# Performance work log

Measured on AMD Instinct MI355X. Metric: run time of the kernel, lower is better.

Reference implementation:

```python
import jax, jax.numpy as jnp
import numpy as np

# Module hyper-parameters (from init_kwargs)
NDIM = 2
KSIZE = [3, 3]            # must be odd per ConvSP checks
DILATION = [0.05, 0.05]
RADIUS = 0.1
C_IN, C_OUT = 64, 64
B, N = 2, 2048


def _offsets():
    # Kernel-cell center offsets relative to the particle, row-major over dims
    # (matches the cartesian ordering of the original C extension).
    axes = [(np.arange(k) - (k - 1) / 2.0) * d for k, d in zip(KSIZE, DILATION)]
    grids = np.meshgrid(*axes, indexing='ij')
    return np.stack([g.reshape(-1) for g in grids], axis=-1).astype(np.float32)  # [ncells, D]


def setup_inputs() -> dict:
    key = jax.random.key(0)
    k1, k2, k3, k4, k5, k6 = jax.random.split(key, 6)
    pos = jax.random.uniform(k1, (B, N, NDIM), dtype=jnp.float32)          # coords in [0,1]^D
    invmass = jax.random.uniform(k2, (B, N), dtype=jnp.float32) * 0.9 + 0.1  # avoid 1/0
    locs = jnp.concatenate([pos, invmass[..., None]], axis=-1)             # [B,N,D+1]
    data = jax.random.normal(k3, (B, C_IN, N), dtype=jnp.float32)
    density = jax.random.uniform(k4, (B, N), dtype=jnp.float32) + 0.5      # strictly positive
    ncells = int(np.prod(KSIZE))
    weight = jax.random.normal(k5, (C_OUT, C_IN, ncells), dtype=jnp.float32) * 0.05
    bias = jax.random.normal(k6, (C_OUT,), dtype=jnp.float32) * 0.05
    return {"locs": locs, "data": data, "density": density, "weight": weight, "bias": bias}


def _convsp(locs, data, density, weight, bias):
    # SPH interpolation at each kernel-cell query point r_{i,k} = x_i + off_k:
    #   field[b,c,i,k] = sum_j (m_j / rho_j) * data[b,c,j] * W(|x_j - r_{i,k}|, RADIUS)
    # with m_j = 1/invmass_j, then a 1x1-style contraction with weight over (c,k).
    pos = locs[..., :NDIM]                               # [B,N,D]
    invmass = locs[..., NDIM]                            # [B,N]
    coef = 1.0 / (invmass * density)                     # m_j / rho_j, [B,N]
    dcoef = data * coef[:, None, :]                      # [B,C,N]
    diff = pos[:, :, None, :] - pos[:, None, :, :]       # x_i - x_j, [B,N,N,D]
    r2 = RADIUS * RADIUS
    knorm = 315.0 / (64.0 * np.pi * RADIUS ** 9)         # poly6 smoothing kernel norm
    offs = _offsets()                                    # [ncells, D]
    bsz, n = pos.shape[0], pos.shape[1]
    out = jnp.broadcast_to(bias[None, :, None], (bsz, weight.shape[0], n))
    for k in range(offs.shape[0]):                       # fixed small ncells=9 loop
        # |x_j - x_i - off| == |(x_i - x_j) + off|
        d2 = jnp.sum((diff + offs[k]) ** 2, axis=-1)     # [B,N,N] (i = query, j = neighbor)
        w = jnp.where(d2 < r2, (r2 - d2) ** 3, 0.0) * knorm
        field = jnp.einsum('bcj,bij->bci', dcoef, w)     # gather-weighted average
        out = out + jnp.einsum('oc,bci->boi', weight[:, :, k], field)
    return out


def reference(locs, data, density, weight, bias):
    return _convsp(locs, data, density, weight, bias)
```

## Files before the change

kernel.cpp:

```cpp
#include <hip/hip_runtime.h>
#include <hip/hip_bf16.h>
#include <stdint.h>

#define BATCH 2
#define NPTS  2048
#define CIN   64
#define COUT  64
#define NCELL 9

#define KNORM 1.5666851e9f
#define R2 0.01f

typedef __attribute__((ext_vector_type(8))) __bf16 bf16x8;
typedef __attribute__((ext_vector_type(4))) float  f32x4;

union B8 { uint4 u; bf16x8 v; };

typedef __attribute__((address_space(3))) uint8_t        lds_t;
typedef const __attribute__((address_space(1))) uint8_t  glb_t;

static __device__ __forceinline__ unsigned pk2(float a, float b) {
    union { __hip_bfloat162 h; unsigned u; } cv;
    cv.h = __float22bfloat162_rn(make_float2(a, b));
    return cv.u;
}


__global__ __launch_bounds__(256) void prep_kernel(
    const float* __restrict__ locs, const float* __restrict__ data,
    const float* __restrict__ density, const float* __restrict__ weight,
    const float* __restrict__ bias,
    float2* __restrict__ posT, uint16_t* __restrict__ dC,
    uint16_t* __restrict__ WB, float* __restrict__ out)
{
    const int tid = threadIdx.x;
    const int g = blockIdx.x;
    if (g < 256) {
        int e = g * 256 + tid;
        int j4 = e & 511, bc = e >> 9;
        int b = bc >> 6;
        float4 dv = *(const float4*)(data + bc * 2048 + j4 * 4);
        float4 de = *(const float4*)(density + b * 2048 + j4 * 4);
        int jb = (b * 2048 + j4 * 4) * 3 + 2;
        float m0 = locs[jb], m1 = locs[jb + 3], m2 = locs[jb + 6], m3 = locs[jb + 9];
        float v0 = dv.x / (m0 * de.x);
        float v1 = dv.y / (m1 * de.y);
        float v2 = dv.z / (m2 * de.z);
        float v3 = dv.w / (m3 * de.w);
        *(uint2*)(dC + bc * 2048 + j4 * 4) = make_uint2(pk2(v0, v1), pk2(v2, v3));
    } else if (g < 272) {
        int jj = (g - 256) * 256 + tid;
        posT[jj] = make_float2(locs[jj * 3], locs[jj * 3 + 1]);
    } else if (g < 272 + NCELL) {
        int cell = g - 272;
        for (int it = 0; it < 16; it++) {
            int e = it * 256 + tid;
            int ks = e >> 11, ob = (e >> 9) & 3, lane = (e >> 3) & 63, jj = e & 7;
            int o = ob * 16 + (lane & 15);
            int c = ks * 32 + ((lane >> 4) & 3) * 8 + jj;
            union { __hip_bfloat16 h; uint16_t u; } cv;
            cv.h = __float2bfloat16(weight[(o * 64 + c) * 9 + cell]);
            WB[cell * 4096 + e] = cv.u;
        }
    } else {
        const int gb = g - (272 + NCELL);
#pragma unroll
        for (int r = 0; r < 2; r++) {
            int e4 = (gb * 512 + r * 256 + tid) * 4;
            float bv = bias[(e4 >> 11) & 63];
            *(float4*)(out + e4) = make_float4(bv, bv, bv, bv);
        }
    }
}

__global__ __launch_bounds__(256, 4) void conv_kernel(
    const float2* __restrict__ posT, const uint16_t* __restrict__ dC,
    const uint16_t* __restrict__ WB, float* __restrict__ out)
{
    __shared__ uint16_t db[2][2048];
    __shared__ float    sft[4 * 16 * 68];

    const int tid  = threadIdx.x;
    const int lane = tid & 63;
    const int wid  = tid >> 6;
    const int cl   = lane & 15;
    const int quad = lane >> 4;
    const int bx   = blockIdx.x;
    const int b    = bx >> 9;
    const int i0   = ((bx >> 2) & 127) * 16;
    const int jh   = bx & 3;
    const int jb0  = jh * 512;

    const int c0 = (wid == 0) ? 0 : (1 + wid * 2);
    const int nc = (wid == 0) ? 3 : 2;
    float oxr[3], oyr[3];
#pragma unroll
    for (int ci = 0; ci < 3; ci++) {
        int k = c0 + (ci < nc ? ci : 0);
        oxr[ci] = (float)(k / 3 - 1) * 0.05f;
        oyr[ci] = (float)(k % 3 - 1) * 0.05f;
    }

    const float2 pI = posT[b * 2048 + i0 + cl];

    f32x4 acc[3][4];
#pragma unroll
    for (int ci = 0; ci < 3; ci++)
#pragma unroll
        for (int nb = 0; nb < 4; nb++) acc[ci][nb] = (f32x4){0.f, 0.f, 0.f, 0.f};

    const uint16_t* srcbase =
        dC + (b * 64 + wid * 16 + (lane >> 2)) * 2048 + jb0 + (lane & 3) * 8;

#define STAGE(n, buf)                                                         \
    __builtin_amdgcn_global_load_lds((glb_t*)(srcbase + (n) * 32),            \
                                     (lds_t*)(&db[buf][wid * 512]), 16, 0, 0)

    STAGE(0, 0);

    for (int n = 0; n < 16; n++) {
        __syncthreads();
        if (n < 15) STAGE(n + 1, (n + 1) & 1);
        const int buf = n & 1;

        B8 bf[4];
#pragma unroll
        for (int nb = 0; nb < 4; nb++)
            bf[nb].u = *(const uint4*)&db[buf][(nb * 16 + cl) * 32 + quad * 8];

        const float4* pp = (const float4*)(posT + b * 2048 + jb0 + n * 32 + quad * 8);
        float4 q0 = pp[0], q1 = pp[1], q2 = pp[2], q3 = pp[3];
        float dxv[8], dyv[8];
        dxv[0] = pI.x - q0.x; dyv[0] = pI.y - q0.y;
        dxv[1] = pI.x - q0.z; dyv[1] = pI.y - q0.w;
        dxv[2] = pI.x - q1.x; dyv[2] = pI.y - q1.y;
        dxv[3] = pI.x - q1.z; dyv[3] = pI.y - q1.w;
        dxv[4] = pI.x - q2.x; dyv[4] = pI.y - q2.y;
        dxv[5] = pI.x - q2.z; dyv[5] = pI.y - q2.w;
        dxv[6] = pI.x - q3.x; dyv[6] = pI.y - q3.y;
        dxv[7] = pI.x - q3.z; dyv[7] = pI.y - q3.w;

#pragma unroll
        for (int ci = 0; ci < 3; ci++) {
            if (ci < nc) {
                float ox = oxr[ci], oy = oyr[ci];
                float w[8];
#pragma unroll
                for (int p = 0; p < 8; p++) {
                    float ax = dxv[p] + ox;
                    float sx = fmaf(-ax, ax, R2);
                    float ay = dyv[p] + oy;
                    float t  = fmaf(-ay, ay, sx);
                    float mt = fmaxf(t, 0.0f);
                    w[p] = (mt * mt) * (mt * KNORM);
                }
                B8 af;
                af.u = make_uint4(pk2(w[0], w[1]), pk2(w[2], w[3]),
                                  pk2(w[4], w[5]), pk2(w[6], w[7]));
#pragma unroll
                for (int nb = 0; nb < 4; nb++)
                    acc[ci][nb] = __builtin_amdgcn_mfma_f32_16x16x32_bf16(
                        af.v, bf[nb].v, acc[ci][nb], 0, 0, 0);
            }
        }
    }

    float* scr = &sft[wid * (16 * 68)];
    f32x4 acc2[4];
#pragma unroll
    for (int ob = 0; ob < 4; ob++) acc2[ob] = (f32x4){0.f, 0.f, 0.f, 0.f};

#pragma unroll
    for (int ci = 0; ci < 3; ci++) {
        if (ci < nc) {
#pragma unroll
            for (int nb = 0; nb < 4; nb++)
#pragma unroll
                for (int r = 0; r < 4; r++)
                    scr[(quad * 4 + r) * 68 + nb * 16 + cl] = acc[ci][nb][r];
            int k = c0 + ci;
#pragma unroll
            for (int ks = 0; ks < 2; ks++) {
                const float* fp = &scr[cl * 68 + ks * 32 + quad * 8];
                float4 lo = *(const float4*)fp;
                float4 hi = *(const float4*)(fp + 4);
                B8 af;
                af.u = make_uint4(pk2(lo.x, lo.y), pk2(lo.z, lo.w),
                                  pk2(hi.x, hi.y), pk2(hi.z, hi.w));
#pragma unroll
                for (int ob = 0; ob < 4; ob++) {
                    B8 wf;
                    wf.u = *(const uint4*)(WB + k * 4096 + (ks * 4 + ob) * 512 + lane * 8);
                    acc2[ob] = __builtin_amdgcn_mfma_f32_16x16x32_bf16(
                        af.v, wf.v, acc2[ob], 0, 0, 0);
                }
            }
        }
    }

    __syncthreads();
#pragma unroll
    for (int ob = 0; ob < 4; ob++)
#pragma unroll
        for (int r = 0; r < 4; r++)
            scr[(quad * 4 + r) * 68 + ob * 16 + cl] = acc2[ob][r];
    __syncthreads();

    {
        const int i  = tid & 15;
        const int og = tid >> 4;
        float4 s0 = *(const float4*)&sft[0 * 1088 + i * 68 + og * 4];
        float4 s1 = *(const float4*)&sft[1 * 1088 + i * 68 + og * 4];
        float4 s2 = *(const float4*)&sft[2 * 1088 + i * 68 + og * 4];
        float4 s3 = *(const float4*)&sft[3 * 1088 + i * 68 + og * 4];
        float v0 = s0.x + s1.x + s2.x + s3.x;
        float v1 = s0.y + s1.y + s2.y + s3.y;
        float v2 = s0.z + s1.z + s2.z + s3.z;
        float v3 = s0.w + s1.w + s2.w + s3.w;
        float* ob_ = out + (b * 64 + og * 4) * 2048 + i0 + i;
        unsafeAtomicAdd(ob_ + 0 * 2048, v0);
        unsafeAtomicAdd(ob_ + 1 * 2048, v1);
        unsafeAtomicAdd(ob_ + 2 * 2048, v2);
        unsafeAtomicAdd(ob_ + 3 * 2048, v3);
    }
#undef STAGE
}

extern "C" void kernel_launch(void* const* d_in, const int* in_sizes, int n_in,
                              void* d_out, int out_size, void* d_ws, size_t ws_size,
                              hipStream_t stream)
{
    const float* locs    = (const float*)d_in[0];
    const float* data    = (const float*)d_in[1];
    const float* density = (const float*)d_in[2];
    const float* weight  = (const float*)d_in[3];
    const float* bias    = (const float*)d_in[4];
    float* out = (float*)d_out;

    float2*   posT = (float2*)d_ws;
    uint16_t* dC   = (uint16_t*)((char*)d_ws + 32768);
    uint16_t* WB   = (uint16_t*)((char*)d_ws + 32768 + 524288);

    prep_kernel<<<272 + NCELL + 128, 256, 0, stream>>>(
        locs, data, density, weight, bias, posT, dC, WB, out);
    conv_kernel<<<BATCH * 128 * 4, 256, 0, stream>>>(posT, dC, WB, out);
}
```

Before: 91.83 us.

## Split neighbor range across waves with all nine cells per wave, drop LDS staging

Restructures the conv kernel so each wave handles all 9 kernel cells over its own slice of the neighbor range, instead of splitting cells across waves. The x-direction distance terms are computed once and shared by three cells each. Neighbor data is now read straight from global memory into registers with a one-step software prefetch, replacing the LDS double buffer with global_load_lds and its per-step barriers. The grid is halved to 2 j-chunks per i-tile and launch bounds drop to 2 blocks per SM. In exchange, register pressure rises sharply from 36 accumulator vectors, the final weight contraction runs 9 cells per wave, and occupancy falls.

After: 93.70 us. +2.0%, slower.

```diff
diff --git a/kernel.cpp b/kernel.cpp
--- a/kernel.cpp
+++ b/kernel.cpp
@@ -15,9 +15,6 @@
 typedef __attribute__((ext_vector_type(4))) float  f32x4;
 
 union B8 { uint4 u; bf16x8 v; };
-
-typedef __attribute__((address_space(3))) uint8_t        lds_t;
-typedef const __attribute__((address_space(1))) uint8_t  glb_t;
 
 static __device__ __forceinline__ unsigned pk2(float a, float b) {
     union { __hip_bfloat162 h; unsigned u; } cv;
@@ -73,12 +70,11 @@
     }
 }
 
-__global__ __launch_bounds__(256, 4) void conv_kernel(
+__global__ __launch_bounds__(256, 2) void conv_kernel(
     const float2* __restrict__ posT, const uint16_t* __restrict__ dC,
     const uint16_t* __restrict__ WB, float* __restrict__ out)
 {
-    __shared__ uint16_t db[2][2048];
-    __shared__ float    sft[4 * 16 * 68];
+    __shared__ float sft[4][16 * 68];
 
     const int tid  = threadIdx.x;
     const int lane = tid & 63;
@@ -86,119 +82,121 @@
     const int cl   = lane & 15;
     const int quad = lane >> 4;
     const int bx   = blockIdx.x;
-    const int b    = bx >> 9;
-    const int i0   = ((bx >> 2) & 127) * 16;
-    const int jh   = bx & 3;
-    const int jb0  = jh * 512;
-
-    const int c0 = (wid == 0) ? 0 : (1 + wid * 2);
-    const int nc = (wid == 0) ? 3 : 2;
-    float oxr[3], oyr[3];
-#pragma unroll
-    for (int ci = 0; ci < 3; ci++) {
-        int k = c0 + (ci < nc ? ci : 0);
-        oxr[ci] = (float)(k / 3 - 1) * 0.05f;
-        oyr[ci] = (float)(k % 3 - 1) * 0.05f;
-    }
+    const int jh   = bx & 1;
+    const int b    = bx >> 8;
+    const int i0   = ((bx >> 1) & 127) * 16;
 
     const float2 pI = posT[b * 2048 + i0 + cl];
 
-    f32x4 acc[3][4];
-#pragma unroll
-    for (int ci = 0; ci < 3; ci++)
-#pragma unroll
-        for (int nb = 0; nb < 4; nb++) acc[ci][nb] = (f32x4){0.f, 0.f, 0.f, 0.f};
-
-    const uint16_t* srcbase =
-        dC + (b * 64 + wid * 16 + (lane >> 2)) * 2048 + jb0 + (lane & 3) * 8;
-
-#define STAGE(n, buf)                                                         \
-    __builtin_amdgcn_global_load_lds((glb_t*)(srcbase + (n) * 32),            \
-                                     (lds_t*)(&db[buf][wid * 512]), 16, 0, 0)
-
-    STAGE(0, 0);
-
-    for (int n = 0; n < 16; n++) {
-        __syncthreads();
-        if (n < 15) STAGE(n + 1, (n + 1) & 1);
-        const int buf = n & 1;
-
-        B8 bf[4];
+    f32x4 acc[NCELL][4];
+#pragma unroll
+    for (int k = 0; k < NCELL; k++)
+#pragma unroll
+        for (int nb = 0; nb < 4; nb++) acc[k][nb] = (f32x4){0.f, 0.f, 0.f, 0.f};
+
+    const uint16_t* rb0 = dC + ((b * 64 +  0 + cl) * 2048) + jh * 1024 + wid * 32 + quad * 8;
+    const uint16_t* rb1 = rb0 + 16 * 2048;
+    const uint16_t* rb2 = rb0 + 32 * 2048;
+    const uint16_t* rb3 = rb0 + 48 * 2048;
+    const float2* pjb = posT + b * 2048 + jh * 1024 + wid * 32 + quad * 8;
+
+    B8 bfc[4];
+    bfc[0].u = *(const uint4*)rb0;
+    bfc[1].u = *(const uint4*)rb1;
+    bfc[2].u = *(const uint4*)rb2;
+    bfc[3].u = *(const uint4*)rb3;
+
+#pragma unroll
+    for (int t = 0; t < 8; t++) {
+        B8 bfn[4];
+        if (t < 7) {
+            bfn[0].u = *(const uint4*)(rb0 + (t + 1) * 128);
+            bfn[1].u = *(const uint4*)(rb1 + (t + 1) * 128);
+            bfn[2].u = *(const uint4*)(rb2 + (t + 1) * 128);
+            bfn[3].u = *(const uint4*)(rb3 + (t + 1) * 128);
+        }
+
+        const float4* pp = (const float4*)(pjb + t * 128);
+        float4 q0 = pp[0], q1 = pp[1], q2 = pp[2], q3 = pp[3];
+        float dyv[8], ru0[8], ru1[8], ru2[8];
+        {
+            float dxv[8];
+            dxv[0] = pI.x - q0.x; dyv[0] = pI.y - q0.y;
+            dxv[1] = pI.x - q0.z; dyv[1] = pI.y - q0.w;
+            dxv[2] = pI.x - q1.x; dyv[2] = pI.y - q1.y;
+            dxv[3] = pI.x - q1.z; dyv[3] = pI.y - q1.w;
+            dxv[4] = pI.x - q2.x; dyv[4] = pI.y - q2.y;
+            dxv[5] = pI.x - q2.z; dyv[5] = pI.y - q2.w;
+            dxv[6] = pI.x - q3.x; dyv[6] = pI.y - q3.y;
+            dxv[7] = pI.x - q3.z; dyv[7] = pI.y - q3.w;
+#pragma unroll
+            for (int p = 0; p < 8; p++) {
+                float a0 = dxv[p] - 0.05f;
+                float a1 = dxv[p];
+                float a2 = dxv[p] + 0.05f;
+                ru0[p] = fmaf(-a0, a0, R2);
+                ru1[p] = fmaf(-a1, a1, R2);
+                ru2[p] = fmaf(-a2, a2, R2);
+            }
+        }
+
+#pragma unroll
+        for (int k = 0; k < NCELL; k++) {
+            const float oy = (float)(k % 3 - 1) * 0.05f;
+            float w[8];
+#pragma unroll
+            for (int p = 0; p < 8; p++) {
+                float ru = (k < 3) ? ru0[p] : (k < 6) ? ru1[p] : ru2[p];
+                float c  = dyv[p] + oy;
+                float tt = fmaf(-c, c, ru);
+                float mt = fmaxf(tt, 0.0f);
+                w[p] = (mt * mt) * (mt * KNORM);
+            }
+            B8 af;
+            af.u = make_uint4(pk2(w[0], w[1]), pk2(w[2], w[3]),
+                              pk2(w[4], w[5]), pk2(w[6], w[7]));
+#pragma unroll
+            for (int nb = 0; nb < 4; nb++)
+                acc[k][nb] = __builtin_amdgcn_mfma_f32_16x16x32_bf16(
+                    af.v, bfc[nb].v, acc[k][nb], 0, 0, 0);
+        }
+
+        if (t < 7) {
+            bfc[0] = bfn[0]; bfc[1] = bfn[1];
+            bfc[2] = bfn[2]; bfc[3] = bfn[3];
+        }
+    }
+
+    float* scr = &sft[wid][0];
+    f32x4 acc2[4];
+#pragma unroll
+    for (int ob = 0; ob < 4; ob++) acc2[ob] = (f32x4){0.f, 0.f, 0.f, 0.f};
+
+#pragma unroll
+    for (int k = 0; k < NCELL; k++) {
 #pragma unroll
         for (int nb = 0; nb < 4; nb++)
-            bf[nb].u = *(const uint4*)&db[buf][(nb * 16 + cl) * 32 + quad * 8];
-
-        const float4* pp = (const float4*)(posT + b * 2048 + jb0 + n * 32 + quad * 8);
-        float4 q0 = pp[0], q1 = pp[1], q2 = pp[2], q3 = pp[3];
-        float dxv[8], dyv[8];
-        dxv[0] = pI.x - q0.x; dyv[0] = pI.y - q0.y;
-        dxv[1] = pI.x - q0.z; dyv[1] = pI.y - q0.w;
-        dxv[2] = pI.x - q1.x; dyv[2] = pI.y - q1.y;
-        dxv[3] = pI.x - q1.z; dyv[3] = pI.y - q1.w;
-        dxv[4] = pI.x - q2.x; dyv[4] = pI.y - q2.y;
-        dxv[5] = pI.x - q2.z; dyv[5] = pI.y - q2.w;
-        dxv[6] = pI.x - q3.x; dyv[6] = pI.y - q3.y;
-        dxv[7] = pI.x - q3.z; dyv[7] = pI.y - q3.w;
-
-#pragma unroll
-        for (int ci = 0; ci < 3; ci++) {
-            if (ci < nc) {
-                float ox = oxr[ci], oy = oyr[ci];
-                float w[8];
-#pragma unroll
-                for (int p = 0; p < 8; p++) {
-                    float ax = dxv[p] + ox;
-                    float sx = fmaf(-ax, ax, R2);
-                    float ay = dyv[p] + oy;
-                    float t  = fmaf(-ay, ay, sx);
-                    float mt = fmaxf(t, 0.0f);
-                    w[p] = (mt * mt) * (mt * KNORM);
-                }
-                B8 af;
-                af.u = make_uint4(pk2(w[0], w[1]), pk2(w[2], w[3]),
-                                  pk2(w[4], w[5]), pk2(w[6], w[7]));
-#pragma unroll
-                for (int nb = 0; nb < 4; nb++)
-                    acc[ci][nb] = __builtin_amdgcn_mfma_f32_16x16x32_bf16(
-                        af.v, bf[nb].v, acc[ci][nb], 0, 0, 0);
+#pragma unroll
+            for (int r = 0; r < 4; r++)
+                scr[(quad * 4 + r) * 68 + nb * 16 + cl] = acc[k][nb][r];
+#pragma unroll
+        for (int ks = 0; ks < 2; ks++) {
+            const float* fp = &scr[cl * 68 + ks * 32 + quad * 8];
+            float4 lo = *(const float4*)fp;
+            float4 hi = *(const float4*)(fp + 4);
+            B8 af;
+            af.u = make_uint4(pk2(lo.x, lo.y), pk2(lo.z, lo.w),
+                              pk2(hi.x, hi.y), pk2(hi.z, hi.w));
+#pragma unroll
+            for (int ob = 0; ob < 4; ob++) {
+                B8 wf;
+                wf.u = *(const uint4*)(WB + k * 4096 + (ks * 4 + ob) * 512 + lane * 8);
+                acc2[ob] = __builtin_amdgcn_mfma_f32_16x16x32_bf16(
+                    af.v, wf.v, acc2[ob], 0, 0, 0);
             }
         }
     }
 
-    float* scr = &sft[wid * (16 * 68)];
-    f32x4 acc2[4];
-#pragma unroll
-    for (int ob = 0; ob < 4; ob++) acc2[ob] = (f32x4){0.f, 0.f, 0.f, 0.f};
-
-#pragma unroll
-    for (int ci = 0; ci < 3; ci++) {
-        if (ci < nc) {
-#pragma unroll
-            for (int nb = 0; nb < 4; nb++)
-#pragma unroll
-                for (int r = 0; r < 4; r++)
-                    scr[(quad * 4 + r) * 68 + nb * 16 + cl] = acc[ci][nb][r];
-            int k = c0 + ci;
-#pragma unroll
-            for (int ks = 0; ks < 2; ks++) {
-                const float* fp = &scr[cl * 68 + ks * 32 + quad * 8];
-                float4 lo = *(const float4*)fp;
-                float4 hi = *(const float4*)(fp + 4);
-                B8 af;
-                af.u = make_uint4(pk2(lo.x, lo.y), pk2(lo.z, lo.w),
-                                  pk2(hi.x, hi.y), pk2(hi.z, hi.w));
-#pragma unroll
-                for (int ob = 0; ob < 4; ob++) {
-                    B8 wf;
-                    wf.u = *(const uint4*)(WB + k * 4096 + (ks * 4 + ob) * 512 + lane * 8);
-                    acc2[ob] = __builtin_amdgcn_mfma_f32_16x16x32_bf16(
-                        af.v, wf.v, acc2[ob], 0, 0, 0);
-                }
-            }
-        }
-    }
-
-    __syncthreads();
 #pragma unroll
     for (int ob = 0; ob < 4; ob++)
 #pragma unroll
@@ -209,21 +207,20 @@
     {
         const int i  = tid & 15;
         const int og = tid >> 4;
-        float4 s0 = *(const float4*)&sft[0 * 1088 + i * 68 + og * 4];
-        float4 s1 = *(const float4*)&sft[1 * 1088 + i * 68 + og * 4];
-        float4 s2 = *(const float4*)&sft[2 * 1088 + i * 68 + og * 4];
-        float4 s3 = *(const float4*)&sft[3 * 1088 + i * 68 + og * 4];
+        float4 s0 = *(const float4*)&sft[0][i * 68 + og * 4];
+        float4 s1 = *(const float4*)&sft[1][i * 68 + og * 4];
+        float4 s2 = *(const float4*)&sft[2][i * 68 + og * 4];
+        float4 s3 = *(const float4*)&sft[3][i * 68 + og * 4];
         float v0 = s0.x + s1.x + s2.x + s3.x;
         float v1 = s0.y + s1.y + s2.y + s3.y;
         float v2 = s0.z + s1.z + s2.z + s3.z;
         float v3 = s0.w + s1.w + s2.w + s3.w;
-        float* ob_ = out + (b * 64 + og * 4) * 2048 + i0 + i;
-        unsafeAtomicAdd(ob_ + 0 * 2048, v0);
-        unsafeAtomicAdd(ob_ + 1 * 2048, v1);
-        unsafeAtomicAdd(ob_ + 2 * 2048, v2);
-        unsafeAtomicAdd(ob_ + 3 * 2048, v3);
-    }
-#undef STAGE
+        float* op = out + (b * 64 + og * 4) * 2048 + i0 + i;
+        unsafeAtomicAdd(op + 0 * 2048, v0);
+        unsafeAtomicAdd(op + 1 * 2048, v1);
+        unsafeAtomicAdd(op + 2 * 2048, v2);
+        unsafeAtomicAdd(op + 3 * 2048, v3);
+    }
 }
 
 extern "C" void kernel_launch(void* const* d_in, const int* in_sizes, int n_in,
@@ -243,5 +240,5 @@
 
     prep_kernel<<<272 + NCELL + 128, 256, 0, stream>>>(
         locs, data, density, weight, bias, posT, dC, WB, out);
-    conv_kernel<<<BATCH * 128 * 4, 256, 0, stream>>>(posT, dC, WB, out);
-}
+    conv_kernel<<<BATCH * 128 * 2, 256, 0, stream>>>(posT, dC, WB, out);
+}
```
